# Optimization experiments

Measured on AMD Instinct MI355X. Metric: run time of the kernel, lower is better.

## Reference

```python
import jax, jax.numpy as jnp
import numpy as np

B, S, D, H, CS = 2, 4096, 1024, 16, 128
HD = D // H            # head_dim = 64
C = S // CS            # num_chunks = 32
NEG = -1e9


def setup_inputs() -> dict:
    key = jax.random.key(0)
    ks = jax.random.split(key, 13)
    w = lambda k: jax.random.normal(k, (D, D), jnp.float32) * 0.02
    b = lambda k: jax.random.normal(k, (D,), jnp.float32) * 0.02
    return {
        'hidden_states': jax.random.normal(ks[0], (B, S, D), jnp.float32),
        'Wq': w(ks[1]), 'bq': b(ks[2]),
        'Wk': w(ks[3]), 'bk': b(ks[4]),
        'Wv': w(ks[5]), 'bv': b(ks[6]),
        'Wo': w(ks[7]), 'bo': b(ks[8]),
        'Wr': w(ks[9]), 'br': b(ks[10]),
        'Wh': w(ks[11]), 'bh': b(ks[12]),
    }


def reference(hidden_states, Wq, bq, Wk, bk, Wv, bv, Wo, bo, Wr, br, Wh, bh):
    scale = 1.0 / np.sqrt(HD)
    proj = lambda x, W, bias: x @ W.T + bias  # torch nn.Linear convention

    # QKV, split heads: [B,H,C,CS,HD]
    def heads(x):
        return x.reshape(B, S, H, HD).transpose(0, 2, 1, 3).reshape(B, H, C, CS, HD)
    qc = heads(proj(hidden_states, Wq, bq))
    kc = heads(proj(hidden_states, Wk, bk))
    vc = heads(proj(hidden_states, Wv, bv))

    # Chunk representation = last token of each chunk (no padding since S % CS == 0)
    chunk_repr = hidden_states.reshape(B, C, CS, D)[:, :, -1, :]  # [B,C,D]
    r = proj(chunk_repr, Wr, br).reshape(B, C, H, HD).transpose(0, 2, 1, 3)  # [B,H,C,HD]
    h = proj(chunk_repr, Wh, bh).reshape(B, C, H, HD).transpose(0, 2, 1, 3)

    # Compressed chunk states F = K^T V per chunk: [B,H,C,HD,HD]
    f = jnp.einsum('bhcsd,bhcse->bhcde', kc, vc)

    # Inter-chunk retrieval (module uses triu mask: chunk i attends chunks j >= i)
    chunk_scores = jnp.einsum('bhcd,bhed->bhce', r, h) * scale  # [B,H,C,C]
    m_out = jnp.triu(jnp.ones((C, C), jnp.float32))
    chunk_scores = jnp.where(m_out == 0, NEG, chunk_scores)
    chunk_probs = jax.nn.softmax(chunk_scores, axis=-1)
    retrieved = jnp.einsum('bhce,bhexy->bhcxy', chunk_probs, f)  # [B,H,C,HD,HD]
    long_term = jnp.einsum('bhcsd,bhcde->bhcse', qc, retrieved)  # [B,H,C,CS,HD]

    # Intra-chunk attention, block-diagonal (mask is triu within chunk)
    local_scores = jnp.einsum('bhcsd,bhctd->bhcst', qc, kc) * scale  # [B,H,C,CS,CS]
    m_in = jnp.triu(jnp.ones((CS, CS), jnp.float32))
    local_scores = jnp.where(m_in == 0, NEG, local_scores)
    local_probs = jax.nn.softmax(local_scores, axis=-1)
    local_out = jnp.einsum('bhcst,bhctd->bhcsd', local_probs, vc)

    out = (long_term + local_out).reshape(B, H, S, HD).transpose(0, 2, 1, 3).reshape(B, S, D)
    return out @ Wo.T + bo
```

## Files before the change

kernel.cpp:

```cpp
#include <hip/hip_runtime.h>
#include <stdint.h>

#define NEG9 (-1e9f)

typedef __attribute__((ext_vector_type(8))) short short8;
typedef __attribute__((ext_vector_type(8))) unsigned short ushort8;
typedef __attribute__((ext_vector_type(4))) unsigned short ushort4_t;
typedef __attribute__((ext_vector_type(4))) float f32x4;

#define MFMA_BF16(a,b,c) __builtin_amdgcn_mfma_f32_16x16x32_bf16((a),(b),(c),0,0,0)

__device__ __forceinline__ unsigned short f2bf(float f) {
  union { float f; unsigned int u; } x; x.f = f;
  unsigned int r = x.u + 0x7fffu + ((x.u >> 16) & 1u);
  return (unsigned short)(r >> 16);
}
__device__ __forceinline__ float bf2f(unsigned short h) {
  union { unsigned int u; float f; } x; x.u = ((unsigned int)h) << 16;
  return x.f;
}
__device__ __forceinline__ void gload_lds16(const unsigned short* g, unsigned short* l) {
  __builtin_amdgcn_global_load_lds(
      (const __attribute__((address_space(1))) unsigned int*)g,
      (__attribute__((address_space(3))) unsigned int*)l, 16, 0, 0);
}

__global__ void cvt_f32_bf16(const float* __restrict__ in, unsigned short* __restrict__ out, int n4) {
  int i = blockIdx.x * blockDim.x + threadIdx.x;
  int stride = gridDim.x * blockDim.x;
  for (; i < n4; i += stride) {
    float4 v = ((const float4*)in)[i];
    ushort4_t o;
    o.x = f2bf(v.x); o.y = f2bf(v.y); o.z = f2bf(v.z); o.w = f2bf(v.w);
    ((ushort4_t*)out)[i] = o;
  }
}

__global__ void cvt_w6(const float* a0, const float* a1, const float* a2,
                       const float* a3, const float* a4, const float* a5,
                       unsigned short* b0, unsigned short* b1, unsigned short* b2,
                       unsigned short* b3, unsigned short* b4, unsigned short* b5) {
  const float* in; unsigned short* out;
  switch (blockIdx.y) {
    case 0: in = a0; out = b0; break;
    case 1: in = a1; out = b1; break;
    case 2: in = a2; out = b2; break;
    case 3: in = a3; out = b3; break;
    case 4: in = a4; out = b4; break;
    default: in = a5; out = b5; break;
  }
  const int n4 = 262144;
  int i = blockIdx.x * blockDim.x + threadIdx.x;
  int stride = gridDim.x * blockDim.x;
  for (; i < n4; i += stride) {
    float4 v = ((const float4*)in)[i];
    ushort4_t o;
    o.x = f2bf(v.x); o.y = f2bf(v.y); o.z = f2bf(v.z); o.w = f2bf(v.w);
    ((ushort4_t*)out)[i] = o;
  }
}

__device__ __forceinline__ void stage_half(const unsigned short* __restrict__ g, int ldg,
                                           unsigned short* lh, int t) {
#pragma unroll
  for (int j = 0; j < 2; j++) {
    int idx = j*512 + t;
    int rowh = idx >> 3;
    int colb = (idx & 7) << 4;
    int scol = colb ^ ((rowh & 7) << 4);
    gload_lds16(g + (long)rowh*ldg + (scol >> 1), lh + idx*8);
  }
}

template<int MODE>
__global__ __launch_bounds__(512, 2)
void gemm8(const unsigned short* __restrict__ A,
           const unsigned short* __restrict__ W,
           const float* __restrict__ b0, const float* __restrict__ b1,
           const float* __restrict__ b2,
           void* __restrict__ o0, void* __restrict__ o1, void* __restrict__ o2,
           int M, int N, int K) {
  __shared__ unsigned short lds[2][2][16384];
  const int t = threadIdx.x;
  const int lane = t & 63;
  const int w = t >> 6;
  const int wm = w >> 2, wn = w & 3;
  const int lr = lane & 15, lp = lane >> 4;

  const int nbn = N >> 8;
  const int nwg = (M >> 8) * nbn;
  int bid = blockIdx.x;
  { int q = nwg >> 3; bid = (bid & 7) * q + (bid >> 3); }
  const int bm = bid / nbn, bn = bid % nbn;
  const long rowA0 = (long)bm << 8;
  const long rowB0 = (long)bn << 8;
  const int KT = K >> 6;

  stage_half(W + rowB0*K,         K, &lds[0][1][0],    t);
  stage_half(W + (rowB0+128)*K,   K, &lds[0][1][8192], t);
  stage_half(A + rowA0*K,         K, &lds[0][0][0],    t);
  stage_half(A + (rowA0+128)*K,   K, &lds[0][0][8192], t);
  if (KT > 1) {
    stage_half(W + rowB0*K + 64,       K, &lds[1][1][0],    t);
    stage_half(W + (rowB0+128)*K + 64, K, &lds[1][1][8192], t);
  }
  asm volatile("s_waitcnt vmcnt(4)" ::: "memory");
  __builtin_amdgcn_s_barrier();

  f32x4 acc[8][4];
#pragma unroll
  for (int m = 0; m < 8; m++)
#pragma unroll
    for (int n = 0; n < 4; n++) acc[m][n] = f32x4{0.f,0.f,0.f,0.f};

  short8 af[4][2], bf0[2][2], bf1[2][2];

  for (int kt = 0; kt < KT; ++kt) {
    const int cur = kt & 1;
    const char* As = (const char*)&lds[cur][0][0];
    const char* Bs = (const char*)&lds[cur][1][0];

#pragma unroll
    for (int mr = 0; mr < 4; mr++) {
      int row = wm*128 + mr*16 + lr;
      int sw = (row & 7) << 4;
#pragma unroll
      for (int kk = 0; kk < 2; kk++)
        af[mr][kk] = *(const short8*)(As + row*128 + ((kk*64 + lp*16) ^ sw));
    }
#pragma unroll
    for (int nr = 0; nr < 2; nr++) {
      int row = wn*64 + nr*16 + lr;
      int sw = (row & 7) << 4;
#pragma unroll
      for (int kk = 0; kk < 2; kk++)
        bf0[nr][kk] = *(const short8*)(Bs + row*128 + ((kk*64 + lp*16) ^ sw));
    }
    if (kt+1 < KT) stage_half(A + rowA0*K + (kt+1)*64, K, &lds[cur^1][0][0], t);
    __builtin_amdgcn_s_barrier();
    __builtin_amdgcn_s_setprio(1);
#pragma unroll
    for (int mr = 0; mr < 4; mr++)
#pragma unroll
      for (int nr = 0; nr < 2; nr++)
#pragma unroll
        for (int kk = 0; kk < 2; kk++)
          acc[mr][nr] = MFMA_BF16(af[mr][kk], bf0[nr][kk], acc[mr][nr]);
    __builtin_amdgcn_s_setprio(0);
    __builtin_amdgcn_s_barrier();

#pragma unroll
    for (int nr = 0; nr < 2; nr++) {
      int row = wn*64 + 32 + nr*16 + lr;
      int sw = (row & 7) << 4;
#pragma unroll
      for (int kk = 0; kk < 2; kk++)
        bf1[nr][kk] = *(const short8*)(Bs + row*128 + ((kk*64 + lp*16) ^ sw));
    }
    if (kt+1 < KT) stage_half(A + (rowA0+128)*K + (kt+1)*64, K, &lds[cur^1][0][8192], t);
    __builtin_amdgcn_s_barrier();
    __builtin_amdgcn_s_setprio(1);
#pragma unroll
    for (int mr = 0; mr < 4; mr++)
#pragma unroll
      for (int nr = 0; nr < 2; nr++)
#pragma unroll
        for (int kk = 0; kk < 2; kk++)
          acc[mr][2+nr] = MFMA_BF16(af[mr][kk], bf1[nr][kk], acc[mr][2+nr]);
    __builtin_amdgcn_s_setprio(0);
    __builtin_amdgcn_s_barrier();

#pragma unroll
    for (int mr = 0; mr < 4; mr++) {
      int row = wm*128 + 64 + mr*16 + lr;
      int sw = (row & 7) << 4;
#pragma unroll
      for (int kk = 0; kk < 2; kk++)
        af[mr][kk] = *(const short8*)(As + row*128 + ((kk*64 + lp*16) ^ sw));
    }
    if (kt+2 < KT) stage_half(W + rowB0*K + (kt+2)*64, K, &lds[cur][1][0], t);
    __builtin_amdgcn_s_barrier();
    __builtin_amdgcn_s_setprio(1);
#pragma unroll
    for (int mr = 0; mr < 4; mr++)
#pragma unroll
      for (int nr = 0; nr < 2; nr++)
#pragma unroll
        for (int kk = 0; kk < 2; kk++)
          acc[4+mr][2+nr] = MFMA_BF16(af[mr][kk], bf1[nr][kk], acc[4+mr][2+nr]);
    __builtin_amdgcn_s_setprio(0);
    __builtin_amdgcn_s_barrier();

    if (kt+2 < KT) stage_half(W + (rowB0+128)*K + (kt+2)*64, K, &lds[cur][1][8192], t);
    __builtin_amdgcn_s_barrier();
    __builtin_amdgcn_s_setprio(1);
#pragma unroll
    for (int mr = 0; mr < 4; mr++)
#pragma unroll
      for (int nr = 0; nr < 2; nr++)
#pragma unroll
        for (int kk = 0; kk < 2; kk++)
          acc[4+mr][nr] = MFMA_BF16(af[mr][kk], bf0[nr][kk], acc[4+mr][nr]);
    __builtin_amdgcn_s_setprio(0);
    if (kt+1 < KT) {
      if (kt+2 < KT) { asm volatile("s_waitcnt vmcnt(4)" ::: "memory"); }
      else           { asm volatile("s_waitcnt vmcnt(0)" ::: "memory"); }
    }
    __builtin_amdgcn_s_barrier();
  }

  if (MODE == 2) {
    const int which = (int)(rowB0 >> 10);
    unsigned short* Co = which==0 ? (unsigned short*)o0 : which==1 ? (unsigned short*)o1 : (unsigned short*)o2;
    const float* bb = which==0 ? b0 : which==1 ? b1 : b2;
    const long colbase = rowB0 - (long)which*1024;
#pragma unroll
    for (int m = 0; m < 8; m++)
#pragma unroll
      for (int n = 0; n < 4; n++) {
        long row = rowA0 + wm*128 + m*16 + lp*4;
        long col = colbase + wn*64 + n*16 + lr;
        float bv = bb[col];
#pragma unroll
        for (int r = 0; r < 4; r++)
          Co[(row + r)*1024 + col] = f2bf(acc[m][n][r] + bv);
      }
  } else {
#pragma unroll
    for (int m = 0; m < 8; m++)
#pragma unroll
      for (int n = 0; n < 4; n++) {
        long row = rowA0 + wm*128 + m*16 + lp*4;
        long col = rowB0 + wn*64 + n*16 + lr;
        float bv = b0[col];
#pragma unroll
        for (int r = 0; r < 4; r++) {
          float v = acc[m][n][r] + bv;
          if (MODE == 1) ((float*)o0)[(row + r)*N + col] = v;
          else ((unsigned short*)o0)[(row + r)*N + col] = f2bf(v);
        }
      }
  }
}

template<int OUT_F32>
__global__ __launch_bounds__(256)
void gemm_bt(const unsigned short* __restrict__ A,
             const unsigned short* __restrict__ W,
             const float* __restrict__ bias,
             void* __restrict__ Cout,
             int M, int N, int K) {
  __shared__ unsigned short As[128*32];
  __shared__ unsigned short Bs[128*32];
  const int t = threadIdx.x;
  const int lane = t & 63;
  const int wave = t >> 6;
  const int wr = wave >> 1, wc = wave & 1;
  const int lr = lane & 15;
  const int lk = (lane >> 4) << 3;

  const int nbn = N >> 7;
  const int nwg = (M >> 7) * nbn;
  int bid = blockIdx.x;
  if ((nwg & 7) == 0) { int q = nwg >> 3; bid = (bid & 7) * q + (bid >> 3); }
  const int bm = bid / nbn, bn = bid % nbn;

  const long rowA0 = (long)bm * 128;
  const long rowB0 = (long)bn * 128;
  const int srow = t >> 2;
  const int scol = (t & 3) << 3;

  f32x4 acc[4][4];
#pragma unroll
  for (int m = 0; m < 4; m++)
#pragma unroll
    for (int n = 0; n < 4; n++) acc[m][n] = f32x4{0.f,0.f,0.f,0.f};

  for (int k0 = 0; k0 < K; k0 += 32) {
    const unsigned short* ga = A + (rowA0 + srow) * K + k0 + scol;
    const unsigned short* gb = W + (rowB0 + srow) * K + k0 + scol;
    gload_lds16(ga,              As + t*8);
    gload_lds16(ga + (long)64*K, As + t*8 + 2048);
    gload_lds16(gb,              Bs + t*8);
    gload_lds16(gb + (long)64*K, Bs + t*8 + 2048);
    __syncthreads();
    short8 af[4], bf[4];
#pragma unroll
    for (int m = 0; m < 4; m++) af[m] = *(const short8*)&As[(wr*64 + m*16 + lr)*32 + lk];
#pragma unroll
    for (int n = 0; n < 4; n++) bf[n] = *(const short8*)&Bs[(wc*64 + n*16 + lr)*32 + lk];
#pragma unroll
    for (int m = 0; m < 4; m++)
#pragma unroll
      for (int n = 0; n < 4; n++)
        acc[m][n] = MFMA_BF16(af[m], bf[n], acc[m][n]);
    __syncthreads();
  }

  const int rg4 = (lane >> 4) * 4;
#pragma unroll
  for (int m = 0; m < 4; m++) {
#pragma unroll
    for (int n = 0; n < 4; n++) {
      long row = rowA0 + wr*64 + m*16 + rg4;
      long col = rowB0 + wc*64 + n*16 + lr;
      float bv = bias[col];
#pragma unroll
      for (int r = 0; r < 4; r++) {
        float v = acc[m][n][r] + bv;
        if (OUT_F32) ((float*)Cout)[(row + r) * N + col] = v;
        else ((unsigned short*)Cout)[(row + r) * N + col] = f2bf(v);
      }
    }
  }
}

__global__ void repr_pad(const float* __restrict__ hs, unsigned short* __restrict__ out,
                         const float* __restrict__ br, const float* __restrict__ bh,
                         float* __restrict__ brh) {
  int r = blockIdx.x;
  int t = threadIdx.x;
  long base = (long)r * 1024;
  if (r < 64) {
    int b = r >> 5, c = r & 31;
    const float* src = hs + ((long)(b*4096 + c*128 + 127)) * 1024;
#pragma unroll
    for (int j = 0; j < 4; j++) { int idx = t + j*256; out[base + idx] = f2bf(src[idx]); }
  } else {
#pragma unroll
    for (int j = 0; j < 4; j++) out[base + t + j*256] = 0;
    if (r == 64) {
#pragma unroll
      for (int j = 0; j < 4; j++) { int idx = t + j*256; brh[idx] = br[idx]; }
    } else if (r == 65) {
#pragma unroll
      for (int j = 0; j < 4; j++) { int idx = t + j*256; brh[1024 + idx] = bh[idx]; }
    }
  }
}

__global__ __launch_bounds__(1024) void chunk_probs_k(
    const unsigned short* __restrict__ rbh,
    float* __restrict__ probs) {
  __shared__ float rt[32][65];
  __shared__ float ht[32][65];
  int h = blockIdx.x, b = blockIdx.y;
  int t = threadIdx.x;
#pragma unroll
  for (int j = 0; j < 2; j++) {
    int idx = t + j*1024;
    int c = idx >> 6, d = idx & 63;
    rt[c][d] = bf2f(rbh[(long)(b*32 + c)*2048 + h*64 + d]);
    ht[c][d] = bf2f(rbh[(long)(b*32 + c)*2048 + 1024 + h*64 + d]);
  }
  __syncthreads();
  int e = t & 31, c = t >> 5;
  float s = 0.f;
#pragma unroll
  for (int d = 0; d < 64; d++) s += rt[c][d] * ht[e][d];
  s *= 0.125f;
  if (e < c) s = NEG9;
  float m = s;
#pragma unroll
  for (int off = 16; off > 0; off >>= 1) m = fmaxf(m, __shfl_xor(m, off, 32));
  float p = __expf(s - m);
  float sum = p;
#pragma unroll
  for (int off = 16; off > 0; off >>= 1) sum += __shfl_xor(sum, off, 32);
  probs[(((long)(b*16 + h))*32 + c)*32 + e] = p / sum;
}

__global__ __launch_bounds__(256) void f_kernel(
    const unsigned short* __restrict__ Kb, const unsigned short* __restrict__ Vb,
    unsigned short* __restrict__ f) {
  __shared__ unsigned short vT[64*136];
  __shared__ unsigned short kT[64*136];
  int bid = blockIdx.x;
  int c = bid & 31, h = (bid >> 5) & 15, b = bid >> 9;
  int t = threadIdx.x;
  const unsigned short* kg = Kb + ((long)(b*4096 + c*128))*1024 + h*64;
  const unsigned short* vg = Vb + ((long)(b*4096 + c*128))*1024 + h*64;
  {
    int eq = t & 7, sq = t >> 3;
    int s0 = sq*4, e0 = eq*8;
    ushort8 v[4], k[4];
#pragma unroll
    for (int r = 0; r < 4; r++) {
      v[r] = *(const ushort8*)&vg[(long)(s0 + r)*1024 + e0];
      k[r] = *(const ushort8*)&kg[(long)(s0 + r)*1024 + e0];
    }
#pragma unroll
    for (int x = 0; x < 8; x++) {
      ushort4_t pv, pk;
      pv.x = v[0][x]; pv.y = v[1][x]; pv.z = v[2][x]; pv.w = v[3][x];
      pk.x = k[0][x]; pk.y = k[1][x]; pk.z = k[2][x]; pk.w = k[3][x];
      *(ushort4_t*)&vT[(e0 + x)*136 + s0] = pv;
      *(ushort4_t*)&kT[(e0 + x)*136 + s0] = pk;
    }
  }
  __syncthreads();
  const int lane = t & 63, w = t >> 6;
  const int lr = lane & 15, lk = (lane >> 4) << 3;
  const int rg4 = (lane >> 4) * 4;
  const int e0w = (w & 1) * 32, d0w = (w >> 1) * 32;

  f32x4 acc[2][2];
#pragma unroll
  for (int m = 0; m < 2; m++)
#pragma unroll
    for (int n = 0; n < 2; n++) acc[m][n] = f32x4{0.f,0.f,0.f,0.f};
#pragma unroll
  for (int kk = 0; kk < 4; kk++) {
    short8 af[2], bf[2];
#pragma unroll
    for (int m = 0; m < 2; m++) af[m] = *(const short8*)&vT[(e0w + m*16 + lr)*136 + kk*32 + lk];
#pragma unroll
    for (int n = 0; n < 2; n++) bf[n] = *(const short8*)&kT[(d0w + n*16 + lr)*136 + kk*32 + lk];
#pragma unroll
    for (int m = 0; m < 2; m++)
#pragma unroll
      for (int n = 0; n < 2; n++) acc[m][n] = MFMA_BF16(af[m], bf[n], acc[m][n]);
  }
  unsigned short* fo = f + (long)bid * 4096;
#pragma unroll
  for (int m = 0; m < 2; m++)
#pragma unroll
    for (int n = 0; n < 2; n++)
#pragma unroll
      for (int r = 0; r < 4; r++)
        fo[(e0w + m*16 + rg4 + r)*64 + d0w + n*16 + lr] = f2bf(acc[m][n][r]);
}

__global__ __launch_bounds__(256) void retrieve_k(
    const float* __restrict__ probs, const unsigned short* __restrict__ f,
    unsigned short* __restrict__ retT) {
  __shared__ float PL[1024];
  int bh = blockIdx.x;
  int xt = blockIdx.y;
  int t = threadIdx.x;
  *(float4*)&PL[t*4] = *(const float4*)&probs[(long)bh*1024 + t*4];
  __syncthreads();
  const unsigned int* fb = (const unsigned int*)(f + (long)bh*32*4096);
  const int xo = xt*256 + t;
  unsigned int fv[32];
#pragma unroll
  for (int ec = 0; ec < 32; ec++) fv[ec] = fb[ec*2048 + xo];
  unsigned int* ro = (unsigned int*)retT + (long)bh*32*2048 + xo;
  for (int c = 0; c < 32; c++) {
    float a0 = 0.f, a1 = 0.f;
#pragma unroll
    for (int e4 = 0; e4 < 8; e4++) {
      float4 p = *(const float4*)&PL[c*32 + e4*4];
#pragma unroll
      for (int j = 0; j < 4; j++) {
        unsigned int v = fv[e4*4 + j];
        union { unsigned int u; float ff; } lo, hi;
        lo.u = v << 16; hi.u = v & 0xffff0000u;
        a0 += p[j] * lo.ff;
        a1 += p[j] * hi.ff;
      }
    }
    ro[(long)c*2048] = (unsigned int)f2bf(a0) | ((unsigned int)f2bf(a1) << 16);
  }
}

__global__ __launch_bounds__(256) void attn_k(
    const unsigned short* __restrict__ Qb,
    const unsigned short* __restrict__ Kb,
    const unsigned short* __restrict__ Vb,
    const unsigned short* __restrict__ retT,
    unsigned short* __restrict__ attn) {
  __shared__ unsigned short ks[128*64];
  __shared__ unsigned short vT[64*136];
  __shared__ unsigned short rT[64*64];
  __shared__ unsigned short P[128*136];
  const int bid = blockIdx.x;
  const int c = bid & 31, h = (bid >> 5) & 15, b = bid >> 9;
  const int t = threadIdx.x;
  const int lane = t & 63, w = t >> 6;
  const int lr = lane & 15, lk = (lane >> 4) << 3;
  const int rg4 = (lane >> 4) * 4;

  const long rowbase = (long)(b*4096 + c*128);
  const unsigned short* kg = Kb + rowbase*1024 + h*64;
  const unsigned short* vg = Vb + rowbase*1024 + h*64;
  const unsigned short* qg = Qb + rowbase*1024 + h*64;
  const unsigned short* rtg = retT + (long)bid*4096;

  {
    const int off = (t & 7) << 4;
#pragma unroll
    for (int i = 0; i < 4; i++) {
      int row = (t >> 3) + i*32;
      int srcoff = off ^ ((row & 7) << 4);
      gload_lds16(kg + (long)row*1024 + (srcoff >> 1), ks + t*8 + i*2048);
    }
#pragma unroll
    for (int i = 0; i < 2; i++) {
      int row = ((t + i*256) >> 3);
      int srcoff = off ^ ((row & 7) << 4);
      gload_lds16(rtg + (long)row*64 + (srcoff >> 1), rT + (t + i*256)*8);
    }
  }
  {
    int eq = t & 7, sq = t >> 3;
    int s0 = sq*4, e0 = eq*8;
    ushort8 v[4];
#pragma unroll
    for (int r = 0; r < 4; r++) v[r] = *(const ushort8*)&vg[(long)(s0 + r)*1024 + e0];
#pragma unroll
    for (int x = 0; x < 8; x++) {
      ushort4_t pv;
      pv.x = v[0][x]; pv.y = v[1][x]; pv.z = v[2][x]; pv.w = v[3][x];
      *(ushort4_t*)&vT[(e0 + x)*136 + s0] = pv;
    }
  }
  __syncthreads();

  short8 qa[2][2];
#pragma unroll
  for (int m = 0; m < 2; m++)
#pragma unroll
    for (int kk = 0; kk < 2; kk++)
      qa[m][kk] = *(const short8*)&qg[(long)(w*32 + m*16 + lr)*1024 + kk*32 + lk];
  f32x4 scf[2][8];
#pragma unroll
  for (int m = 0; m < 2; m++)
#pragma unroll
    for (int n = 0; n < 8; n++) scf[m][n] = f32x4{0.f,0.f,0.f,0.f};
#pragma unroll
  for (int n = 0; n < 8; n++) {
    const int krow = n*16 + lr;
    const int swzmask = (krow & 7) << 4;
#pragma unroll
    for (int kk = 0; kk < 2; kk++) {
      int colb = (kk*64 + ((lane >> 4) << 4)) ^ swzmask;
      short8 kf = *(const short8*)&ks[krow*64 + (colb >> 1)];
#pragma unroll
      for (int m = 0; m < 2; m++) scf[m][n] = MFMA_BF16(qa[m][kk], kf, scf[m][n]);
    }
  }

  float rsum[2][4];
#pragma unroll
  for (int m = 0; m < 2; m++) {
#pragma unroll
    for (int r = 0; r < 4; r++) {
      int srow = w*32 + m*16 + rg4 + r;
      float vals[8];
      float mx = -1e30f;
#pragma unroll
      for (int n = 0; n < 8; n++) {
        int tcol = n*16 + lr;
        float v_ = scf[m][n][r] * 0.125f;
        if (tcol < srow) v_ = NEG9;
        vals[n] = v_;
        mx = fmaxf(mx, v_);
      }
#pragma unroll
      for (int off = 1; off < 16; off <<= 1) mx = fmaxf(mx, __shfl_xor(mx, off, 16));
      float sum = 0.f;
#pragma unroll
      for (int n = 0; n < 8; n++) {
        float p = __expf(vals[n] - mx);
        sum += p;
        P[srow*136 + n*16 + lr] = f2bf(p);
      }
#pragma unroll
      for (int off = 1; off < 16; off <<= 1) sum += __shfl_xor(sum, off, 16);
      rsum[m][r] = sum;
    }
  }

  f32x4 outa[2][4];
#pragma unroll
  for (int m = 0; m < 2; m++)
#pragma unroll
    for (int n = 0; n < 4; n++) outa[m][n] = f32x4{0.f,0.f,0.f,0.f};
#pragma unroll
  for (int n = 0; n < 4; n++) {
    const int rrow = n*16 + lr;
    const int swzmask = (rrow & 7) << 4;
#pragma unroll
    for (int kk = 0; kk < 2; kk++) {
      int colb = (kk*64 + ((lane >> 4) << 4)) ^ swzmask;
      short8 rf = *(const short8*)&rT[rrow*64 + (colb >> 1)];
#pragma unroll
      for (int m = 0; m < 2; m++) outa[m][n] = MFMA_BF16(qa[m][kk], rf, outa[m][n]);
    }
  }

  f32x4 pv[2][4];
#pragma unroll
  for (int m = 0; m < 2; m++)
#pragma unroll
    for (int n = 0; n < 4; n++) pv[m][n] = f32x4{0.f,0.f,0.f,0.f};
#pragma unroll
  for (int kk = 0; kk < 4; kk++) {
    short8 pa[2];
#pragma unroll
    for (int m = 0; m < 2; m++) pa[m] = *(const short8*)&P[(w*32 + m*16 + lr)*136 + kk*32 + lk];
#pragma unroll
    for (int n = 0; n < 4; n++) {
      short8 vf = *(const short8*)&vT[(n*16 + lr)*136 + kk*32 + lk];
#pragma unroll
      for (int m = 0; m < 2; m++) pv[m][n] = MFMA_BF16(pa[m], vf, pv[m][n]);
    }
  }

  unsigned short* ao = attn + rowbase*1024 + h*64;
#pragma unroll
  for (int m = 0; m < 2; m++)
#pragma unroll
    for (int n = 0; n < 4; n++)
#pragma unroll
      for (int r = 0; r < 4; r++) {
        int srow = w*32 + m*16 + rg4 + r;
        float v_ = pv[m][n][r] / rsum[m][r] + outa[m][n][r];
        ao[(long)srow*1024 + n*16 + lr] = f2bf(v_);
      }
}

extern "C" void kernel_launch(void* const* d_in, const int* in_sizes, int n_in,
                              void* d_out, int out_size, void* d_ws, size_t ws_size,
                              hipStream_t stream) {
  const float* hs = (const float*)d_in[0];
  const float* Wq = (const float*)d_in[1];
  const float* bq = (const float*)d_in[2];
  const float* Wk = (const float*)d_in[3];
  const float* bk = (const float*)d_in[4];
  const float* Wv = (const float*)d_in[5];
  const float* bv = (const float*)d_in[6];
  const float* Wo = (const float*)d_in[7];
  const float* bo = (const float*)d_in[8];
  const float* Wr = (const float*)d_in[9];
  const float* br = (const float*)d_in[10];
  const float* Wh = (const float*)d_in[11];
  const float* bh = (const float*)d_in[12];

  char* p = (char*)d_ws;
  unsigned short* hsb  = (unsigned short*)p; p += (size_t)8192*1024*2;
  unsigned short* Wqkv = (unsigned short*)p; p += (size_t)3072*1024*2;
  unsigned short* Wob  = (unsigned short*)p; p += (size_t)1024*1024*2;
  unsigned short* Wrh  = (unsigned short*)p; p += (size_t)2048*1024*2;
  unsigned short* Qb   = (unsigned short*)p; p += (size_t)8192*1024*2;
  unsigned short* Kb   = (unsigned short*)p; p += (size_t)8192*1024*2;
  unsigned short* Vb   = (unsigned short*)p; p += (size_t)8192*1024*2;
  unsigned short* reprb= (unsigned short*)p; p += (size_t)128*1024*2;
  unsigned short* rbhb = (unsigned short*)p; p += (size_t)128*2048*2;
  float*          brh  = (float*)p;          p += (size_t)2048*4;
  float*          probs= (float*)p;          p += (size_t)2*16*32*32*4;
  unsigned short* fbuf = (unsigned short*)p; p += (size_t)2*16*32*4096*2;
  unsigned short* retT = (unsigned short*)p; p += (size_t)2*16*32*4096*2;
  unsigned short* attnb = hsb;

  cvt_f32_bf16<<<8192, 256, 0, stream>>>(hs, hsb, 2097152);
  cvt_w6<<<dim3(256, 6), 256, 0, stream>>>(Wq, Wk, Wv, Wo, Wr, Wh,
                                           Wqkv, Wqkv + (size_t)1024*1024,
                                           Wqkv + (size_t)2048*1024,
                                           Wob, Wrh, Wrh + (size_t)1024*1024);
  repr_pad<<<128, 256, 0, stream>>>(hs, reprb, br, bh, brh);

  gemm8<2><<<384, 512, 0, stream>>>(hsb, Wqkv, bq, bk, bv, Qb, Kb, Vb, 8192, 3072, 1024);

  gemm_bt<0><<<16, 256, 0, stream>>>(reprb, Wrh, brh, rbhb, 128, 2048, 1024);

  chunk_probs_k<<<dim3(16, 2), 1024, 0, stream>>>(rbhb, probs);
  f_kernel<<<1024, 256, 0, stream>>>(Kb, Vb, fbuf);
  retrieve_k<<<dim3(32, 8), 256, 0, stream>>>(probs, fbuf, retT);
  attn_k<<<1024, 256, 0, stream>>>(Qb, Kb, Vb, retT, attnb);

  gemm8<1><<<128, 512, 0, stream>>>(attnb, Wob, bo, nullptr, nullptr,
                                    d_out, nullptr, nullptr, 8192, 1024, 1024);
}
```

Baseline: 289.8 us.

## Shrink gemm8 N-tile from 256 to 128 to double workgroup count

The gemm8 tile changes from 256x256 to 256x128. The LDS layout, accumulator count, MFMA phase structure (four sub-phases become two per k-step) and wait counts are rewritten to match, and the QKV and output GEMMs launch twice as many blocks. The aim is better CU occupancy and load balance, since the old grids (384 and 128 blocks) underfill 256 CUs. In exchange, arithmetic intensity per block drops and more A-tile traffic is needed.

```diff
diff --git a/kernel.cpp b/kernel.cpp
--- a/kernel.cpp
+++ b/kernel.cpp
@@ -80,45 +80,45 @@
            const float* __restrict__ b2,
            void* __restrict__ o0, void* __restrict__ o1, void* __restrict__ o2,
            int M, int N, int K) {
-  __shared__ unsigned short lds[2][2][16384];
+  __shared__ unsigned short lds[2][24576];
   const int t = threadIdx.x;
   const int lane = t & 63;
   const int w = t >> 6;
   const int wm = w >> 2, wn = w & 3;
   const int lr = lane & 15, lp = lane >> 4;
 
-  const int nbn = N >> 8;
+  const int nbn = N >> 7;
   const int nwg = (M >> 8) * nbn;
   int bid = blockIdx.x;
   { int q = nwg >> 3; bid = (bid & 7) * q + (bid >> 3); }
   const int bm = bid / nbn, bn = bid % nbn;
   const long rowA0 = (long)bm << 8;
-  const long rowB0 = (long)bn << 8;
+  const long rowB0 = (long)bn << 7;
   const int KT = K >> 6;
 
-  stage_half(W + rowB0*K,         K, &lds[0][1][0],    t);
-  stage_half(W + (rowB0+128)*K,   K, &lds[0][1][8192], t);
-  stage_half(A + rowA0*K,         K, &lds[0][0][0],    t);
-  stage_half(A + (rowA0+128)*K,   K, &lds[0][0][8192], t);
+  stage_half(W + rowB0*K,         K, &lds[0][16384], t);
+  stage_half(A + rowA0*K,         K, &lds[0][0],     t);
+  stage_half(A + (rowA0+128)*K,   K, &lds[0][8192],  t);
   if (KT > 1) {
-    stage_half(W + rowB0*K + 64,       K, &lds[1][1][0],    t);
-    stage_half(W + (rowB0+128)*K + 64, K, &lds[1][1][8192], t);
-  }
-  asm volatile("s_waitcnt vmcnt(4)" ::: "memory");
+    stage_half(W + rowB0*K + 64,  K, &lds[1][16384], t);
+    asm volatile("s_waitcnt vmcnt(2)" ::: "memory");
+  } else {
+    asm volatile("s_waitcnt vmcnt(0)" ::: "memory");
+  }
   __builtin_amdgcn_s_barrier();
 
-  f32x4 acc[8][4];
+  f32x4 acc[8][2];
 #pragma unroll
   for (int m = 0; m < 8; m++)
 #pragma unroll
-    for (int n = 0; n < 4; n++) acc[m][n] = f32x4{0.f,0.f,0.f,0.f};
-
-  short8 af[4][2], bf0[2][2], bf1[2][2];
+    for (int n = 0; n < 2; n++) acc[m][n] = f32x4{0.f,0.f,0.f,0.f};
+
+  short8 af[4][2], bf[2][2];
 
   for (int kt = 0; kt < KT; ++kt) {
     const int cur = kt & 1;
-    const char* As = (const char*)&lds[cur][0][0];
-    const char* Bs = (const char*)&lds[cur][1][0];
+    const char* As = (const char*)&lds[cur][0];
+    const char* Bs = (const char*)&lds[cur][16384];
 
 #pragma unroll
     for (int mr = 0; mr < 4; mr++) {
@@ -130,13 +130,16 @@
     }
 #pragma unroll
     for (int nr = 0; nr < 2; nr++) {
-      int row = wn*64 + nr*16 + lr;
+      int row = wn*32 + nr*16 + lr;
       int sw = (row & 7) << 4;
 #pragma unroll
       for (int kk = 0; kk < 2; kk++)
-        bf0[nr][kk] = *(const short8*)(Bs + row*128 + ((kk*64 + lp*16) ^ sw));
-    }
-    if (kt+1 < KT) stage_half(A + rowA0*K + (kt+1)*64, K, &lds[cur^1][0][0], t);
+        bf[nr][kk] = *(const short8*)(Bs + row*128 + ((kk*64 + lp*16) ^ sw));
+    }
+    if (kt+1 < KT) {
+      stage_half(A + rowA0*K + (kt+1)*64,         K, &lds[cur^1][0],    t);
+      stage_half(A + (rowA0+128)*K + (kt+1)*64,   K, &lds[cur^1][8192], t);
+    }
     __builtin_amdgcn_s_barrier();
     __builtin_amdgcn_s_setprio(1);
 #pragma unroll
@@ -145,28 +148,7 @@
       for (int nr = 0; nr < 2; nr++)
 #pragma unroll
         for (int kk = 0; kk < 2; kk++)
-          acc[mr][nr] = MFMA_BF16(af[mr][kk], bf0[nr][kk], acc[mr][nr]);
-    __builtin_amdgcn_s_setprio(0);
-    __builtin_amdgcn_s_barrier();
-
-#pragma unroll
-    for (int nr = 0; nr < 2; nr++) {
-      int row = wn*64 + 32 + nr*16 + lr;
-      int sw = (row & 7) << 4;
-#pragma unroll
-      for (int kk = 0; kk < 2; kk++)
-        bf1[nr][kk] = *(const short8*)(Bs + row*128 + ((kk*64 + lp*16) ^ sw));
-    }
-    if (kt+1 < KT) stage_half(A + (rowA0+128)*K + (kt+1)*64, K, &lds[cur^1][0][8192], t);
-    __builtin_amdgcn_s_barrier();
-    __builtin_amdgcn_s_setprio(1);
-#pragma unroll
-    for (int mr = 0; mr < 4; mr++)
-#pragma unroll
-      for (int nr = 0; nr < 2; nr++)
-#pragma unroll
-        for (int kk = 0; kk < 2; kk++)
-          acc[mr][2+nr] = MFMA_BF16(af[mr][kk], bf1[nr][kk], acc[mr][2+nr]);
+          acc[mr][nr] = MFMA_BF16(af[mr][kk], bf[nr][kk], acc[mr][nr]);
     __builtin_amdgcn_s_setprio(0);
     __builtin_amdgcn_s_barrier();
 
@@ -178,7 +160,7 @@
       for (int kk = 0; kk < 2; kk++)
         af[mr][kk] = *(const short8*)(As + row*128 + ((kk*64 + lp*16) ^ sw));
     }
-    if (kt+2 < KT) stage_half(W + rowB0*K + (kt+2)*64, K, &lds[cur][1][0], t);
+    if (kt+2 < KT) stage_half(W + rowB0*K + (kt+2)*64, K, &lds[cur][16384], t);
     __builtin_amdgcn_s_barrier();
     __builtin_amdgcn_s_setprio(1);
 #pragma unroll
@@ -187,23 +169,10 @@
       for (int nr = 0; nr < 2; nr++)
 #pragma unroll
         for (int kk = 0; kk < 2; kk++)
-          acc[4+mr][2+nr] = MFMA_BF16(af[mr][kk], bf1[nr][kk], acc[4+mr][2+nr]);
-    __builtin_amdgcn_s_setprio(0);
-    __builtin_amdgcn_s_barrier();
-
-    if (kt+2 < KT) stage_half(W + (rowB0+128)*K + (kt+2)*64, K, &lds[cur][1][8192], t);
-    __builtin_amdgcn_s_barrier();
-    __builtin_amdgcn_s_setprio(1);
-#pragma unroll
-    for (int mr = 0; mr < 4; mr++)
-#pragma unroll
-      for (int nr = 0; nr < 2; nr++)
-#pragma unroll
-        for (int kk = 0; kk < 2; kk++)
-          acc[4+mr][nr] = MFMA_BF16(af[mr][kk], bf0[nr][kk], acc[4+mr][nr]);
+          acc[4+mr][nr] = MFMA_BF16(af[mr][kk], bf[nr][kk], acc[4+mr][nr]);
     __builtin_amdgcn_s_setprio(0);
     if (kt+1 < KT) {
-      if (kt+2 < KT) { asm volatile("s_waitcnt vmcnt(4)" ::: "memory"); }
+      if (kt+2 < KT) { asm volatile("s_waitcnt vmcnt(2)" ::: "memory"); }
       else           { asm volatile("s_waitcnt vmcnt(0)" ::: "memory"); }
     }
     __builtin_amdgcn_s_barrier();
@@ -217,9 +186,9 @@
 #pragma unroll
     for (int m = 0; m < 8; m++)
 #pragma unroll
-      for (int n = 0; n < 4; n++) {
+      for (int n = 0; n < 2; n++) {
         long row = rowA0 + wm*128 + m*16 + lp*4;
-        long col = colbase + wn*64 + n*16 + lr;
+        long col = colbase + wn*32 + n*16 + lr;
         float bv = bb[col];
 #pragma unroll
         for (int r = 0; r < 4; r++)
@@ -229,9 +198,9 @@
 #pragma unroll
     for (int m = 0; m < 8; m++)
 #pragma unroll
-      for (int n = 0; n < 4; n++) {
+      for (int n = 0; n < 2; n++) {
         long row = rowA0 + wm*128 + m*16 + lp*4;
-        long col = rowB0 + wn*64 + n*16 + lr;
+        long col = rowB0 + wn*32 + n*16 + lr;
         float bv = b0[col];
 #pragma unroll
         for (int r = 0; r < 4; r++) {
@@ -661,7 +630,7 @@
                                            Wob, Wrh, Wrh + (size_t)1024*1024);
   repr_pad<<<128, 256, 0, stream>>>(hs, reprb, br, bh, brh);
 
-  gemm8<2><<<384, 512, 0, stream>>>(hsb, Wqkv, bq, bk, bv, Qb, Kb, Vb, 8192, 3072, 1024);
+  gemm8<2><<<768, 512, 0, stream>>>(hsb, Wqkv, bq, bk, bv, Qb, Kb, Vb, 8192, 3072, 1024);
 
   gemm_bt<0><<<16, 256, 0, stream>>>(reprb, Wrh, brh, rbhb, 128, 2048, 1024);
 
@@ -670,6 +639,6 @@
   retrieve_k<<<dim3(32, 8), 256, 0, stream>>>(probs, fbuf, retT);
   attn_k<<<1024, 256, 0, stream>>>(Qb, Kb, Vb, retT, attnb);
 
-  gemm8<1><<<128, 512, 0, stream>>>(attnb, Wob, bo, nullptr, nullptr,
+  gemm8<1><<<256, 512, 0, stream>>>(attnb, Wob, bo, nullptr, nullptr,
                                     d_out, nullptr, nullptr, 8192, 1024, 1024);
 }
```

Measured after the change: 276.1 us. -4.7%, faster.

## Add 256x128-tile GEMM for output projection and remap warp tiles in QKV GEMM

Applied to the files above, without the earlier changes.

The old 256x256 GEMM is renamed gemm256 and its warp-to-subtile mapping changes so each wave covers interleaved 64x32 quadrants of the four LDS halves. Its wait counts are retuned and one barrier is dropped. A new gemm8 uses 256x128 tiles with a smaller LDS footprint and runs the output projection on 256 workgroups instead of 128, so all CUs get work. The costs are lower per-block reuse of A in the new kernel and a risk of races from the changed waitcnt and barrier placement.

```diff
diff --git a/kernel.cpp b/kernel.cpp
--- a/kernel.cpp
+++ b/kernel.cpp
@@ -74,12 +74,12 @@
 
 template<int MODE>
 __global__ __launch_bounds__(512, 2)
-void gemm8(const unsigned short* __restrict__ A,
-           const unsigned short* __restrict__ W,
-           const float* __restrict__ b0, const float* __restrict__ b1,
-           const float* __restrict__ b2,
-           void* __restrict__ o0, void* __restrict__ o1, void* __restrict__ o2,
-           int M, int N, int K) {
+void gemm256(const unsigned short* __restrict__ A,
+             const unsigned short* __restrict__ W,
+             const float* __restrict__ b0, const float* __restrict__ b1,
+             const float* __restrict__ b2,
+             void* __restrict__ o0, void* __restrict__ o1, void* __restrict__ o2,
+             int M, int N, int K) {
   __shared__ unsigned short lds[2][2][16384];
   const int t = threadIdx.x;
   const int lane = t & 63;
@@ -103,8 +103,10 @@
   if (KT > 1) {
     stage_half(W + rowB0*K + 64,       K, &lds[1][1][0],    t);
     stage_half(W + (rowB0+128)*K + 64, K, &lds[1][1][8192], t);
-  }
-  asm volatile("s_waitcnt vmcnt(4)" ::: "memory");
+    asm volatile("s_waitcnt vmcnt(6)" ::: "memory");
+  } else {
+    asm volatile("s_waitcnt vmcnt(2)" ::: "memory");
+  }
   __builtin_amdgcn_s_barrier();
 
   f32x4 acc[8][4];
@@ -122,7 +124,7 @@
 
 #pragma unroll
     for (int mr = 0; mr < 4; mr++) {
-      int row = wm*128 + mr*16 + lr;
+      int row = wm*64 + mr*16 + lr;
       int sw = (row & 7) << 4;
 #pragma unroll
       for (int kk = 0; kk < 2; kk++)
@@ -130,7 +132,7 @@
     }
 #pragma unroll
     for (int nr = 0; nr < 2; nr++) {
-      int row = wn*64 + nr*16 + lr;
+      int row = wn*32 + nr*16 + lr;
       int sw = (row & 7) << 4;
 #pragma unroll
       for (int kk = 0; kk < 2; kk++)
@@ -151,11 +153,11 @@
 
 #pragma unroll
     for (int nr = 0; nr < 2; nr++) {
-      int row = wn*64 + 32 + nr*16 + lr;
+      int row = wn*32 + nr*16 + lr;
       int sw = (row & 7) << 4;
 #pragma unroll
       for (int kk = 0; kk < 2; kk++)
-        bf1[nr][kk] = *(const short8*)(Bs + row*128 + ((kk*64 + lp*16) ^ sw));
+        bf1[nr][kk] = *(const short8*)(Bs + 16384 + row*128 + ((kk*64 + lp*16) ^ sw));
     }
     if (kt+1 < KT) stage_half(A + (rowA0+128)*K + (kt+1)*64, K, &lds[cur^1][0][8192], t);
     __builtin_amdgcn_s_barrier();
@@ -168,15 +170,17 @@
         for (int kk = 0; kk < 2; kk++)
           acc[mr][2+nr] = MFMA_BF16(af[mr][kk], bf1[nr][kk], acc[mr][2+nr]);
     __builtin_amdgcn_s_setprio(0);
+    if (kt+1 < KT) { asm volatile("s_waitcnt vmcnt(8)" ::: "memory"); }
+    else           { asm volatile("s_waitcnt vmcnt(0)" ::: "memory"); }
     __builtin_amdgcn_s_barrier();
 
 #pragma unroll
     for (int mr = 0; mr < 4; mr++) {
-      int row = wm*128 + 64 + mr*16 + lr;
+      int row = wm*64 + mr*16 + lr;
       int sw = (row & 7) << 4;
 #pragma unroll
       for (int kk = 0; kk < 2; kk++)
-        af[mr][kk] = *(const short8*)(As + row*128 + ((kk*64 + lp*16) ^ sw));
+        af[mr][kk] = *(const short8*)(As + 16384 + row*128 + ((kk*64 + lp*16) ^ sw));
     }
     if (kt+2 < KT) stage_half(W + rowB0*K + (kt+2)*64, K, &lds[cur][1][0], t);
     __builtin_amdgcn_s_barrier();
@@ -192,7 +196,6 @@
     __builtin_amdgcn_s_barrier();
 
     if (kt+2 < KT) stage_half(W + (rowB0+128)*K + (kt+2)*64, K, &lds[cur][1][8192], t);
-    __builtin_amdgcn_s_barrier();
     __builtin_amdgcn_s_setprio(1);
 #pragma unroll
     for (int mr = 0; mr < 4; mr++)
@@ -203,8 +206,8 @@
           acc[4+mr][nr] = MFMA_BF16(af[mr][kk], bf0[nr][kk], acc[4+mr][nr]);
     __builtin_amdgcn_s_setprio(0);
     if (kt+1 < KT) {
-      if (kt+2 < KT) { asm volatile("s_waitcnt vmcnt(4)" ::: "memory"); }
-      else           { asm volatile("s_waitcnt vmcnt(0)" ::: "memory"); }
+      if (kt+2 < KT) { asm volatile("s_waitcnt vmcnt(6)" ::: "memory"); }
+      else           { asm volatile("s_waitcnt vmcnt(2)" ::: "memory"); }
     }
     __builtin_amdgcn_s_barrier();
   }
@@ -218,8 +221,8 @@
     for (int m = 0; m < 8; m++)
 #pragma unroll
       for (int n = 0; n < 4; n++) {
-        long row = rowA0 + wm*128 + m*16 + lp*4;
-        long col = colbase + wn*64 + n*16 + lr;
+        long row = rowA0 + (m>>2)*128 + wm*64 + (m&3)*16 + lp*4;
+        long col = colbase + (n>>1)*128 + wn*32 + (n&1)*16 + lr;
         float bv = bb[col];
 #pragma unroll
         for (int r = 0; r < 4; r++)
@@ -230,8 +233,148 @@
     for (int m = 0; m < 8; m++)
 #pragma unroll
       for (int n = 0; n < 4; n++) {
+        long row = rowA0 + (m>>2)*128 + wm*64 + (m&3)*16 + lp*4;
+        long col = rowB0 + (n>>1)*128 + wn*32 + (n&1)*16 + lr;
+        float bv = b0[col];
+#pragma unroll
+        for (int r = 0; r < 4; r++) {
+          float v = acc[m][n][r] + bv;
+          if (MODE == 1) ((float*)o0)[(row + r)*N + col] = v;
+          else ((unsigned short*)o0)[(row + r)*N + col] = f2bf(v);
+        }
+      }
+  }
+}
+
+template<int MODE>
+__global__ __launch_bounds__(512, 2)
+void gemm8(const unsigned short* __restrict__ A,
+           const unsigned short* __restrict__ W,
+           const float* __restrict__ b0, const float* __restrict__ b1,
+           const float* __restrict__ b2,
+           void* __restrict__ o0, void* __restrict__ o1, void* __restrict__ o2,
+           int M, int N, int K) {
+  __shared__ unsigned short lds[2][24576];
+  const int t = threadIdx.x;
+  const int lane = t & 63;
+  const int w = t >> 6;
+  const int wm = w >> 2, wn = w & 3;
+  const int lr = lane & 15, lp = lane >> 4;
+
+  const int nbn = N >> 7;
+  const int nwg = (M >> 8) * nbn;
+  int bid = blockIdx.x;
+  { int q = nwg >> 3; bid = (bid & 7) * q + (bid >> 3); }
+  const int bm = bid / nbn, bn = bid % nbn;
+  const long rowA0 = (long)bm << 8;
+  const long rowB0 = (long)bn << 7;
+  const int KT = K >> 6;
+
+  stage_half(W + rowB0*K,         K, &lds[0][16384], t);
+  stage_half(A + rowA0*K,         K, &lds[0][0],     t);
+  stage_half(A + (rowA0+128)*K,   K, &lds[0][8192],  t);
+  if (KT > 1) {
+    stage_half(W + rowB0*K + 64,  K, &lds[1][16384], t);
+    asm volatile("s_waitcnt vmcnt(2)" ::: "memory");
+  } else {
+    asm volatile("s_waitcnt vmcnt(0)" ::: "memory");
+  }
+  __builtin_amdgcn_s_barrier();
+
+  f32x4 acc[8][2];
+#pragma unroll
+  for (int m = 0; m < 8; m++)
+#pragma unroll
+    for (int n = 0; n < 2; n++) acc[m][n] = f32x4{0.f,0.f,0.f,0.f};
+
+  short8 af[4][2], bf[2][2];
+
+  for (int kt = 0; kt < KT; ++kt) {
+    const int cur = kt & 1;
+    const char* As = (const char*)&lds[cur][0];
+    const char* Bs = (const char*)&lds[cur][16384];
+
+#pragma unroll
+    for (int mr = 0; mr < 4; mr++) {
+      int row = wm*128 + mr*16 + lr;
+      int sw = (row & 7) << 4;
+#pragma unroll
+      for (int kk = 0; kk < 2; kk++)
+        af[mr][kk] = *(const short8*)(As + row*128 + ((kk*64 + lp*16) ^ sw));
+    }
+#pragma unroll
+    for (int nr = 0; nr < 2; nr++) {
+      int row = wn*32 + nr*16 + lr;
+      int sw = (row & 7) << 4;
+#pragma unroll
+      for (int kk = 0; kk < 2; kk++)
+        bf[nr][kk] = *(const short8*)(Bs + row*128 + ((kk*64 + lp*16) ^ sw));
+    }
+    if (kt+1 < KT) {
+      stage_half(A + rowA0*K + (kt+1)*64,         K, &lds[cur^1][0],    t);
+      stage_half(A + (rowA0+128)*K + (kt+1)*64,   K, &lds[cur^1][8192], t);
+    }
+    __builtin_amdgcn_s_barrier();
+    __builtin_amdgcn_s_setprio(1);
+#pragma unroll
+    for (int mr = 0; mr < 4; mr++)
+#pragma unroll
+      for (int nr = 0; nr < 2; nr++)
+#pragma unroll
+        for (int kk = 0; kk < 2; kk++)
+          acc[mr][nr] = MFMA_BF16(af[mr][kk], bf[nr][kk], acc[mr][nr]);
+    __builtin_amdgcn_s_setprio(0);
+    __builtin_amdgcn_s_barrier();
+
+#pragma unroll
+    for (int mr = 0; mr < 4; mr++) {
+      int row = wm*128 + 64 + mr*16 + lr;
+      int sw = (row & 7) << 4;
+#pragma unroll
+      for (int kk = 0; kk < 2; kk++)
+        af[mr][kk] = *(const short8*)(As + row*128 + ((kk*64 + lp*16) ^ sw));
+    }
+    if (kt+2 < KT) stage_half(W + rowB0*K + (kt+2)*64, K, &lds[cur][16384], t);
+    __builtin_amdgcn_s_barrier();
+    __builtin_amdgcn_s_setprio(1);
+#pragma unroll
+    for (int mr = 0; mr < 4; mr++)
+#pragma unroll
+      for (int nr = 0; nr < 2; nr++)
+#pragma unroll
+        for (int kk = 0; kk < 2; kk++)
+          acc[4+mr][nr] = MFMA_BF16(af[mr][kk], bf[nr][kk], acc[4+mr][nr]);
+    __builtin_amdgcn_s_setprio(0);
+    if (kt+1 < KT) {
+      if (kt+2 < KT) { asm volatile("s_waitcnt vmcnt(2)" ::: "memory"); }
+      else           { asm volatile("s_waitcnt vmcnt(0)" ::: "memory"); }
+    }
+    __builtin_amdgcn_s_barrier();
+  }
+
+  if (MODE == 2) {
+    const int which = (int)(rowB0 >> 10);
+    unsigned short* Co = which==0 ? (unsigned short*)o0 : which==1 ? (unsigned short*)o1 : (unsigned short*)o2;
+    const float* bb = which==0 ? b0 : which==1 ? b1 : b2;
+    const long colbase = rowB0 - (long)which*1024;
+#pragma unroll
+    for (int m = 0; m < 8; m++)
+#pragma unroll
+      for (int n = 0; n < 2; n++) {
         long row = rowA0 + wm*128 + m*16 + lp*4;
-        long col = rowB0 + wn*64 + n*16 + lr;
+        long col = colbase + wn*32 + n*16 + lr;
+        float bv = bb[col];
+#pragma unroll
+        for (int r = 0; r < 4; r++)
+          Co[(row + r)*1024 + col] = f2bf(acc[m][n][r] + bv);
+      }
+  } else {
+#pragma unroll
+    for (int m = 0; m < 8; m++)
+#pragma unroll
+      for (int n = 0; n < 2; n++) {
+        long row = rowA0 + wm*128 + m*16 + lp*4;
+        long col = rowB0 + wn*32 + n*16 + lr;
         float bv = b0[col];
 #pragma unroll
         for (int r = 0; r < 4; r++) {
@@ -661,7 +804,7 @@
                                            Wob, Wrh, Wrh + (size_t)1024*1024);
   repr_pad<<<128, 256, 0, stream>>>(hs, reprb, br, bh, brh);
 
-  gemm8<2><<<384, 512, 0, stream>>>(hsb, Wqkv, bq, bk, bv, Qb, Kb, Vb, 8192, 3072, 1024);
+  gemm256<2><<<384, 512, 0, stream>>>(hsb, Wqkv, bq, bk, bv, Qb, Kb, Vb, 8192, 3072, 1024);
 
   gemm_bt<0><<<16, 256, 0, stream>>>(reprb, Wrh, brh, rbhb, 128, 2048, 1024);
 
@@ -670,6 +813,6 @@
   retrieve_k<<<dim3(32, 8), 256, 0, stream>>>(probs, fbuf, retT);
   attn_k<<<1024, 256, 0, stream>>>(Qb, Kb, Vb, retT, attnb);
 
-  gemm8<1><<<128, 512, 0, stream>>>(attnb, Wob, bo, nullptr, nullptr,
+  gemm8<1><<<256, 512, 0, stream>>>(attnb, Wob, bo, nullptr, nullptr,
                                     d_out, nullptr, nullptr, 8192, 1024, 1024);
 }
```

After: 276.3 us. 4.7% less time.
